# Kernel optimization log

Measured on AMD Instinct MI355X. Metric: run time of the kernel, lower is better.

Reference implementation:

```python
import jax, jax.numpy as jnp
import numpy as np

N_QUBITS = 4
N_FEATURES = 16
B = 1048576


def _bcast(theta):
    # theta: scalar or [B]; make broadcastable against [B,2,2,2] amp slices
    return theta if jnp.ndim(theta) == 0 else theta.reshape(theta.shape[0], 1, 1, 1)


def apply_ry(state, theta, w):
    # state: [B,2,2,2,2] complex; RY(theta) on wire w
    th = _bcast(theta)
    c = jnp.cos(th / 2).astype(state.dtype)
    s = jnp.sin(th / 2).astype(state.dtype)
    st = jnp.moveaxis(state, w + 1, -1)
    a0, a1 = st[..., 0], st[..., 1]
    st = jnp.stack([c * a0 - s * a1, s * a0 + c * a1], axis=-1)
    return jnp.moveaxis(st, -1, w + 1)


def apply_rz(state, theta, w):
    # RZ(theta) = diag(e^{-i theta/2}, e^{+i theta/2}) on wire w
    th = _bcast(theta)
    ph = jnp.exp(-0.5j * th.astype(jnp.float32)).astype(state.dtype)
    st = jnp.moveaxis(state, w + 1, -1)
    a0, a1 = st[..., 0], st[..., 1]
    st = jnp.stack([ph * a0, jnp.conj(ph) * a1], axis=-1)
    return jnp.moveaxis(st, -1, w + 1)


def cnot(state, c, t):
    st = jnp.moveaxis(state, (c + 1, t + 1), (-2, -1))  # [...,2(ctrl),2(tgt)]
    st = jnp.stack([st[..., 0, :], st[..., 1, ::-1]], axis=-2)
    return jnp.moveaxis(st, (-2, -1), (c + 1, t + 1))


def quantum_encoder_batched(x, qw):
    # x: [B,16] float32, qw: [8] float32 -> latents [B,4] (PauliZ expvals)
    b = x.shape[0]
    state = jnp.zeros((b, 16), jnp.complex64).at[:, 0].set(1.0)
    state = state.reshape(b, 2, 2, 2, 2)
    pi = jnp.float32(np.pi)
    for i in range(N_QUBITS):
        state = apply_ry(state, x[:, i] * pi, i)
        state = apply_rz(state, x[:, i + N_QUBITS] * pi, i)
    for i in range(N_QUBITS - 1):
        state = cnot(state, i, i + 1)
    for i in range(N_QUBITS):
        state = apply_ry(state, qw[2 * i], i)
        state = apply_rz(state, qw[2 * i + 1], i)
    for i in range(N_QUBITS - 1):
        state = cnot(state, i, i + 1)
    probs = state.real ** 2 + state.imag ** 2  # [B,2,2,2,2]
    zs = []
    for i in range(N_QUBITS):
        axes = tuple(a for a in range(1, N_QUBITS + 1) if a != i + 1)
        p = probs.sum(axes)  # [B,2]
        zs.append(p[:, 0] - p[:, 1])
    return jnp.stack(zs, axis=1)  # [B,4]


def setup_inputs() -> dict:
    key = jax.random.key(0)
    ks = jax.random.split(key, 8)
    x = jax.random.uniform(ks[0], (B, N_FEATURES), dtype=jnp.float32)
    q_weights = 0.01 * jax.random.normal(ks[1], (2 * N_QUBITS,), dtype=jnp.float32)
    # decoder: Linear(4,16) -> ReLU -> Linear(16,32) -> ReLU -> Linear(32,16)
    W1 = jax.random.normal(ks[2], (16, 4), dtype=jnp.float32) / jnp.sqrt(4.0)
    b1 = jnp.zeros((16,), jnp.float32)
    W2 = jax.random.normal(ks[3], (32, 16), dtype=jnp.float32) / jnp.sqrt(16.0)
    b2 = jnp.zeros((32,), jnp.float32)
    W3 = jax.random.normal(ks[4], (16, 32), dtype=jnp.float32) / jnp.sqrt(32.0)
    b3 = jnp.zeros((16,), jnp.float32)
    return {"x": x, "q_weights": q_weights, "W1": W1, "b1": b1,
            "W2": W2, "b2": b2, "W3": W3, "b3": b3}


def reference(x, q_weights, W1, b1, W2, b2, W3, b3):
    z = quantum_encoder_batched(x, q_weights)          # [B,4]
    h = jax.nn.relu(z @ W1.T + b1)                      # [B,16]
    h = jax.nn.relu(h @ W2.T + b2)                      # [B,32]
    return h @ W3.T + b3                                # [B,16]
```

## Files before the change

### kernel.cpp

```cpp
#include <hip/hip_runtime.h>

using u16 = unsigned short;
using u32 = unsigned int;
typedef float v2f   __attribute__((ext_vector_type(2)));
typedef float f32x4 __attribute__((ext_vector_type(4)));
typedef short s16x8 __attribute__((ext_vector_type(8)));

union FragU { u32 d[4]; s16x8 s; };

__device__ __forceinline__ u32 rne16(u32 u) { return (u + 0x7FFFu + ((u >> 16) & 1u)) >> 16; }
__device__ __forceinline__ u32 pk_bf16(float a, float b) {
    return rne16(__float_as_uint(a)) | (rne16(__float_as_uint(b)) << 16);
}
__device__ __forceinline__ void split2(float w0, float w1, u32& hi, u32& lo) {
    u32 u0 = __float_as_uint(w0), u1 = __float_as_uint(w1);
    hi = (u0 >> 16) | (u1 & 0xFFFF0000u);
    float r0 = w0 - __uint_as_float(u0 & 0xFFFF0000u);
    float r1 = w1 - __uint_as_float(u1 & 0xFFFF0000u);
    lo = pk_bf16(r0, r1);
}
__device__ __forceinline__ u32 bp(int ib, u32 v) {
    return (u32)__builtin_amdgcn_ds_bpermute(ib, (int)v);
}
__device__ __forceinline__ v2f pkfma(v2f a, v2f b, v2f c) { return __builtin_elementwise_fma(a, b, c); }
__device__ __forceinline__ v2f s2v(float x) { return (v2f){x, x}; }
__device__ __forceinline__ f32x4 tov(float4 v) { return (f32x4){v.x, v.y, v.z, v.w}; }
#define MFMA16 __builtin_amdgcn_mfma_f32_16x16x32_bf16

__global__ void __launch_bounds__(256) qae_bperm(
    const float* __restrict__ x,  const float* __restrict__ qw,
    const float* __restrict__ W1, const float* __restrict__ b1,
    const float* __restrict__ W2, const float* __restrict__ b2,
    const float* __restrict__ W3, const float* __restrict__ b3,
    float* __restrict__ out, int n)
{
    int tid  = threadIdx.x;
    int b    = blockIdx.x * 256 + tid;
    int bc   = b < n ? b : n - 1;
    int lane = tid & 63;
    int vn   = lane & 15, vq = lane >> 4;
    int gbase = blockIdx.x * 256 + (tid - lane);

    const float4* xf = reinterpret_cast<const float4*>(x);
    float4 xa = xf[(size_t)bc * 4];
    float4 xc = xf[(size_t)bc * 4 + 1];

    float th[4] = { xa.x, xa.y, xa.z, xa.w };
    float ph[4] = { xc.x, xc.y, xc.z, xc.w };
    float u0r[4], u0i[4], u1r[4], u1i[4];
    #pragma unroll
    for (int i = 0; i < 4; ++i) {
        float ct = __builtin_amdgcn_cosf(th[i] * 0.25f);
        float st = __builtin_amdgcn_sinf(th[i] * 0.25f);
        float cp = __builtin_amdgcn_cosf(ph[i] * 0.25f);
        float sp = __builtin_amdgcn_sinf(ph[i] * 0.25f);
        u0r[i] = ct * cp;  u0i[i] = -ct * sp;
        u1r[i] = st * cp;  u1i[i] = st * sp;
    }
    float p01r[4], p01i[4], p23r[4], p23i[4];
    #pragma unroll
    for (int a = 0; a < 2; ++a)
        #pragma unroll
        for (int c = 0; c < 2; ++c) {
            float arq = a ? u1r[0] : u0r[0], aiq = a ? u1i[0] : u0i[0];
            float brq = c ? u1r[1] : u0r[1], biq = c ? u1i[1] : u0i[1];
            p01r[a*2+c] = arq*brq - aiq*biq;
            p01i[a*2+c] = arq*biq + aiq*brq;
            float crq = a ? u1r[2] : u0r[2], ciq = a ? u1i[2] : u0i[2];
            float drq = c ? u1r[3] : u0r[3], diq = c ? u1i[3] : u0i[3];
            p23r[a*2+c] = crq*drq - ciq*diq;
            p23i[a*2+c] = crq*diq + ciq*drq;
        }
    v2f amp[16];
    #pragma unroll
    for (int i = 0; i < 16; ++i) {
        int q0i=(i>>3)&1, q1i=(i>>2)&1, q2i=(i>>1)&1, q3i=i&1;
        int g = (q0i<<3) | ((q1i^q0i)<<2) | ((q2i^q1i)<<1) | (q3i^q2i);
        int hi = g >> 2, lo = g & 3;
        amp[i] = (v2f){ p01r[hi]*p23r[lo] - p01i[hi]*p23i[lo],
                        p01r[hi]*p23i[lo] + p01i[hi]*p23r[lo] };
    }
    const float INV4PI = 0.07957747154594767f;
    #pragma unroll
    for (int w = 0; w < 4; ++w) {
        float a = qw[2 * w];
        v2f vc = s2v(__builtin_amdgcn_cosf(a * INV4PI));
        v2f vs = s2v(__builtin_amdgcn_sinf(a * INV4PI));
        int stride = 1 << (3 - w);
        #pragma unroll
        for (int m = 0; m < 16; ++m) {
            if (m & stride) continue;
            int i0 = m, i1 = m | stride;
            v2f a0 = amp[i0], a1 = amp[i1];
            amp[i0] = pkfma(vc, a0, -(vs * a1));
            amp[i1] = pkfma(vc, a1,  (vs * a0));
        }
    }
    float p[16];
    #pragma unroll
    for (int i = 0; i < 16; ++i) {
        int q0i=(i>>3)&1, q1i=(i>>2)&1, q2i=(i>>1)&1, q3i=i&1;
        int g = (q0i<<3) | ((q1i^q0i)<<2) | ((q2i^q1i)<<1) | (q3i^q2i);
        v2f q = amp[g] * amp[g];
        p[i] = q.x + q.y;
    }
    float s2a[8], s4[4];
    #pragma unroll
    for (int j = 0; j < 8; ++j) s2a[j] = p[2*j] + p[2*j+1];
    #pragma unroll
    for (int j = 0; j < 4; ++j) s4[j] = s2a[2*j] + s2a[2*j+1];
    float zv0 = (s4[0] + s4[1]) - (s4[2] + s4[3]);
    float zv1 = (s4[0] - s4[1]) + (s4[2] - s4[3]);
    float zv2 = (s2a[0]-s2a[1]) + (s2a[2]-s2a[3]) + (s2a[4]-s2a[5]) + (s2a[6]-s2a[7]);
    float zv3 = (p[0]-p[1]) + (p[2]-p[3]) + (p[4]-p[5]) + (p[6]-p[7])
              + (p[8]-p[9]) + (p[10]-p[11]) + (p[12]-p[13]) + (p[14]-p[15]);

    u32 zd0 = pk_bf16(zv0, zv1);
    u32 zd1 = pk_bf16(zv2, zv3);

    bool q0 = (vq == 0), qlt2 = (vq < 2);
    FragU A1h, A1l;
    {
        float4 w = reinterpret_cast<const float4*>(W1)[vn];
        u32 h0,l0,h1,l1; split2(w.x, w.y, h0, l0); split2(w.z, w.w, h1, l1);
        A1h.d[0] = q0 ? h0 : 0; A1h.d[1] = q0 ? h1 : 0; A1h.d[2] = 0; A1h.d[3] = 0;
        A1l.d[0] = q0 ? l0 : 0; A1l.d[1] = q0 ? l1 : 0; A1l.d[2] = 0; A1l.d[3] = 0;
    }
    FragU A2ah, A2al, A2bh, A2bl, A3h, A3l;
    {
        const float4* p0 = reinterpret_cast<const float4*>(W2 + vn * 16 + (vq & 1) * 8);
        const float4* p1 = reinterpret_cast<const float4*>(W2 + (16 + vn) * 16 + (vq & 1) * 8);
        float4 a0 = p0[0], a1 = p0[1], c0 = p1[0], c1 = p1[1];
        u32 h, l;
        split2(a0.x,a0.y,h,l); A2ah.d[0]=qlt2?h:0; A2al.d[0]=qlt2?l:0;
        split2(a0.z,a0.w,h,l); A2ah.d[1]=qlt2?h:0; A2al.d[1]=qlt2?l:0;
        split2(a1.x,a1.y,h,l); A2ah.d[2]=qlt2?h:0; A2al.d[2]=qlt2?l:0;
        split2(a1.z,a1.w,h,l); A2ah.d[3]=qlt2?h:0; A2al.d[3]=qlt2?l:0;
        split2(c0.x,c0.y,h,l); A2bh.d[0]=qlt2?h:0; A2bl.d[0]=qlt2?l:0;
        split2(c0.z,c0.w,h,l); A2bh.d[1]=qlt2?h:0; A2bl.d[1]=qlt2?l:0;
        split2(c1.x,c1.y,h,l); A2bh.d[2]=qlt2?h:0; A2bl.d[2]=qlt2?l:0;
        split2(c1.z,c1.w,h,l); A2bh.d[3]=qlt2?h:0; A2bl.d[3]=qlt2?l:0;
        const float4* p3 = reinterpret_cast<const float4*>(W3 + vn * 32 + vq * 8);
        float4 e0 = p3[0], e1 = p3[1];
        split2(e0.x,e0.y,h,l); A3h.d[0]=h; A3l.d[0]=l;
        split2(e0.z,e0.w,h,l); A3h.d[1]=h; A3l.d[1]=l;
        split2(e1.x,e1.y,h,l); A3h.d[2]=h; A3l.d[2]=l;
        split2(e1.z,e1.w,h,l); A3h.d[3]=h; A3l.d[3]=l;
    }
    float4 c1b = reinterpret_cast<const float4*>(b1)[vq];
    float4 c2b0 = reinterpret_cast<const float4*>(b2)[vq];
    float4 c2b1 = reinterpret_cast<const float4*>(b2)[4 + vq];
    float4 c3b = reinterpret_cast<const float4*>(b3)[vq];

    int i2a = ((((2 * vq)    ) & 3) * 16 + vn) * 4;
    int i2b = ((((2 * vq) + 1) & 3) * 16 + vn) * 4;

    #pragma unroll
    for (int t = 0; t < 4; ++t) {
        int viL = (t * 16 + vn) * 4;
        FragU B1; B1.d[0] = bp(viL, zd0); B1.d[1] = bp(viL, zd1); B1.d[2] = 0; B1.d[3] = 0;
        f32x4 c1 = tov(c1b);
        c1 = MFMA16(A1l.s, B1.s, c1, 0, 0, 0);
        c1 = MFMA16(A1h.s, B1.s, c1, 0, 0, 0);
        u32 da0 = pk_bf16(fmaxf(c1[0], 0.f), fmaxf(c1[1], 0.f));
        u32 da1 = pk_bf16(fmaxf(c1[2], 0.f), fmaxf(c1[3], 0.f));

        FragU B2;
        B2.d[0] = bp(i2a, da0); B2.d[1] = bp(i2a, da1);
        B2.d[2] = bp(i2b, da0); B2.d[3] = bp(i2b, da1);
        f32x4 ca = tov(c2b0), cb = tov(c2b1);
        ca = MFMA16(A2al.s, B2.s, ca, 0, 0, 0);
        ca = MFMA16(A2ah.s, B2.s, ca, 0, 0, 0);
        cb = MFMA16(A2bl.s, B2.s, cb, 0, 0, 0);
        cb = MFMA16(A2bh.s, B2.s, cb, 0, 0, 0);
        u32 ea0 = pk_bf16(fmaxf(ca[0],0.f), fmaxf(ca[1],0.f));
        u32 ea1 = pk_bf16(fmaxf(ca[2],0.f), fmaxf(ca[3],0.f));
        u32 eb0 = pk_bf16(fmaxf(cb[0],0.f), fmaxf(cb[1],0.f));
        u32 eb1 = pk_bf16(fmaxf(cb[2],0.f), fmaxf(cb[3],0.f));

        u32 s0a = bp(i2a, ea0), s0b = bp(i2a, eb0);
        u32 s1a = bp(i2a, ea1), s1b = bp(i2a, eb1);
        u32 s2_ = bp(i2b, ea0), s2b = bp(i2b, eb0);
        u32 s3a = bp(i2b, ea1), s3b = bp(i2b, eb1);
        FragU B3;
        B3.d[0] = qlt2 ? s0a : s0b;
        B3.d[1] = qlt2 ? s1a : s1b;
        B3.d[2] = qlt2 ? s2_ : s2b;
        B3.d[3] = qlt2 ? s3a : s3b;
        f32x4 c3 = tov(c3b);
        c3 = MFMA16(A3l.s, B3.s, c3, 0, 0, 0);
        c3 = MFMA16(A3h.s, B3.s, c3, 0, 0, 0);

        int R = gbase + t * 16 + vn;
        if (R < n)
            *reinterpret_cast<float4*>(out + (size_t)R * 16 + vq * 4) =
                make_float4(c3[0], c3[1], c3[2], c3[3]);
    }
}

extern "C" void kernel_launch(void* const* d_in, const int* in_sizes, int n_in,
                              void* d_out, int out_size, void* d_ws, size_t ws_size,
                              hipStream_t stream) {
    const float* x  = (const float*)d_in[0];
    const float* qw = (const float*)d_in[1];
    const float* W1 = (const float*)d_in[2];
    const float* b1 = (const float*)d_in[3];
    const float* W2 = (const float*)d_in[4];
    const float* b2 = (const float*)d_in[5];
    const float* W3 = (const float*)d_in[6];
    const float* b3 = (const float*)d_in[7];
    float* out = (float*)d_out;

    int n = in_sizes[0] / 16;
    int blocks = (n + 255) / 256;
    qae_bperm<<<blocks, 256, 0, stream>>>(x, qw, W1, b1, W2, b2, W3, b3, out, n);
}
```

Measured before the change: 133.7 us.

## Share weight-fragment prep via LDS, simplify encoder maths, use hardware bf16 convert

Each wave now prepares one pair of the bf16 hi/lo split weight fragments and stores them in shared memory. After a barrier every wave reads all fragments back, instead of each wave loading and splitting all weights itself. The product-state construction uses the fact that the RZ phase on |0> cancels globally, so the zero-imaginary terms are dropped. The probability reduction is done on packed v2f, and the software round-to-nearest bf16 packing is replaced with the v_cvt_pk_bf16_f32 instruction. The cost is added LDS traffic and a block-wide barrier, with some risk of small numerical differences.

Result: faster. 126.6 us (-5.3%).

```diff
diff --git a/kernel.cpp b/kernel.cpp
--- a/kernel.cpp
+++ b/kernel.cpp
@@ -6,18 +6,19 @@
 typedef float f32x4 __attribute__((ext_vector_type(4)));
 typedef short s16x8 __attribute__((ext_vector_type(8)));
 
-union FragU { u32 d[4]; s16x8 s; };
-
-__device__ __forceinline__ u32 rne16(u32 u) { return (u + 0x7FFFu + ((u >> 16) & 1u)) >> 16; }
-__device__ __forceinline__ u32 pk_bf16(float a, float b) {
-    return rne16(__float_as_uint(a)) | (rne16(__float_as_uint(b)) << 16);
+union FragU { u32 d[4]; s16x8 s; uint4 q; };
+
+__device__ __forceinline__ u32 cvt_pk_bf16(float a, float b) {
+    u32 r;
+    asm("v_cvt_pk_bf16_f32 %0, %1, %2" : "=v"(r) : "v"(a), "v"(b));
+    return r;
 }
 __device__ __forceinline__ void split2(float w0, float w1, u32& hi, u32& lo) {
     u32 u0 = __float_as_uint(w0), u1 = __float_as_uint(w1);
     hi = (u0 >> 16) | (u1 & 0xFFFF0000u);
     float r0 = w0 - __uint_as_float(u0 & 0xFFFF0000u);
     float r1 = w1 - __uint_as_float(u1 & 0xFFFF0000u);
-    lo = pk_bf16(r0, r1);
+    lo = cvt_pk_bf16(r0, r1);
 }
 __device__ __forceinline__ u32 bp(int ib, u32 v) {
     return (u32)__builtin_amdgcn_ds_bpermute(ib, (int)v);
@@ -38,47 +39,92 @@
     int b    = blockIdx.x * 256 + tid;
     int bc   = b < n ? b : n - 1;
     int lane = tid & 63;
+    int wid  = tid >> 6;
     int vn   = lane & 15, vq = lane >> 4;
     int gbase = blockIdx.x * 256 + (tid - lane);
+
+    __shared__ uint4 shfrag[8][64];
 
     const float4* xf = reinterpret_cast<const float4*>(x);
     float4 xa = xf[(size_t)bc * 4];
     float4 xc = xf[(size_t)bc * 4 + 1];
 
-    float th[4] = { xa.x, xa.y, xa.z, xa.w };
-    float ph[4] = { xc.x, xc.y, xc.z, xc.w };
-    float u0r[4], u0i[4], u1r[4], u1i[4];
+    bool q0 = (vq == 0), qlt2 = (vq < 2);
+
+    if (wid == 0) {
+        float4 w = reinterpret_cast<const float4*>(W1)[vn];
+        u32 h0, l0, h1, l1; split2(w.x, w.y, h0, l0); split2(w.z, w.w, h1, l1);
+        shfrag[0][lane] = make_uint4(q0 ? h0 : 0, q0 ? h1 : 0, 0, 0);
+        shfrag[1][lane] = make_uint4(q0 ? l0 : 0, q0 ? l1 : 0, 0, 0);
+    } else if (wid == 1) {
+        const float4* p0 = reinterpret_cast<const float4*>(W2 + vn * 16 + (vq & 1) * 8);
+        float4 a0 = p0[0], a1 = p0[1];
+        u32 h, l; uint4 H, L;
+        split2(a0.x, a0.y, h, l); H.x = qlt2 ? h : 0; L.x = qlt2 ? l : 0;
+        split2(a0.z, a0.w, h, l); H.y = qlt2 ? h : 0; L.y = qlt2 ? l : 0;
+        split2(a1.x, a1.y, h, l); H.z = qlt2 ? h : 0; L.z = qlt2 ? l : 0;
+        split2(a1.z, a1.w, h, l); H.w = qlt2 ? h : 0; L.w = qlt2 ? l : 0;
+        shfrag[2][lane] = H; shfrag[3][lane] = L;
+    } else if (wid == 2) {
+        const float4* p1 = reinterpret_cast<const float4*>(W2 + (16 + vn) * 16 + (vq & 1) * 8);
+        float4 c0 = p1[0], c1v = p1[1];
+        u32 h, l; uint4 H, L;
+        split2(c0.x, c0.y, h, l); H.x = qlt2 ? h : 0; L.x = qlt2 ? l : 0;
+        split2(c0.z, c0.w, h, l); H.y = qlt2 ? h : 0; L.y = qlt2 ? l : 0;
+        split2(c1v.x, c1v.y, h, l); H.z = qlt2 ? h : 0; L.z = qlt2 ? l : 0;
+        split2(c1v.z, c1v.w, h, l); H.w = qlt2 ? h : 0; L.w = qlt2 ? l : 0;
+        shfrag[4][lane] = H; shfrag[5][lane] = L;
+    } else {
+        const float4* p3 = reinterpret_cast<const float4*>(W3 + vn * 32 + vq * 8);
+        float4 e0 = p3[0], e1 = p3[1];
+        u32 h, l; uint4 H, L;
+        split2(e0.x, e0.y, h, l); H.x = h; L.x = l;
+        split2(e0.z, e0.w, h, l); H.y = h; L.y = l;
+        split2(e1.x, e1.y, h, l); H.z = h; L.z = l;
+        split2(e1.z, e1.w, h, l); H.w = h; L.w = l;
+        shfrag[6][lane] = H; shfrag[7][lane] = L;
+    }
+
+    float th[4]  = { xa.x, xa.y, xa.z, xa.w };
+    float phv[4] = { xc.x, xc.y, xc.z, xc.w };
+    float c4[4], u1r[4], u1i[4];
     #pragma unroll
     for (int i = 0; i < 4; ++i) {
-        float ct = __builtin_amdgcn_cosf(th[i] * 0.25f);
-        float st = __builtin_amdgcn_sinf(th[i] * 0.25f);
-        float cp = __builtin_amdgcn_cosf(ph[i] * 0.25f);
-        float sp = __builtin_amdgcn_sinf(ph[i] * 0.25f);
-        u0r[i] = ct * cp;  u0i[i] = -ct * sp;
-        u1r[i] = st * cp;  u1i[i] = st * sp;
+        float c  = __builtin_amdgcn_cosf(th[i]  * 0.25f);
+        float s  = __builtin_amdgcn_sinf(th[i]  * 0.25f);
+        float cz = __builtin_amdgcn_cosf(phv[i] * 0.5f);
+        float sz = __builtin_amdgcn_sinf(phv[i] * 0.5f);
+        c4[i] = c; u1r[i] = s * cz; u1i[i] = s * sz;
     }
     float p01r[4], p01i[4], p23r[4], p23i[4];
-    #pragma unroll
-    for (int a = 0; a < 2; ++a)
-        #pragma unroll
-        for (int c = 0; c < 2; ++c) {
-            float arq = a ? u1r[0] : u0r[0], aiq = a ? u1i[0] : u0i[0];
-            float brq = c ? u1r[1] : u0r[1], biq = c ? u1i[1] : u0i[1];
-            p01r[a*2+c] = arq*brq - aiq*biq;
-            p01i[a*2+c] = arq*biq + aiq*brq;
-            float crq = a ? u1r[2] : u0r[2], ciq = a ? u1i[2] : u0i[2];
-            float drq = c ? u1r[3] : u0r[3], diq = c ? u1i[3] : u0i[3];
-            p23r[a*2+c] = crq*drq - ciq*diq;
-            p23i[a*2+c] = crq*diq + ciq*drq;
-        }
+    p01r[0] = c4[0] * c4[1];                          p01i[0] = 0.f;
+    p01r[1] = c4[0] * u1r[1];                         p01i[1] = c4[0] * u1i[1];
+    p01r[2] = u1r[0] * c4[1];                         p01i[2] = u1i[0] * c4[1];
+    p01r[3] = u1r[0] * u1r[1] - u1i[0] * u1i[1];
+    p01i[3] = u1r[0] * u1i[1] + u1i[0] * u1r[1];
+    p23r[0] = c4[2] * c4[3];                          p23i[0] = 0.f;
+    p23r[1] = c4[2] * u1r[3];                         p23i[1] = c4[2] * u1i[3];
+    p23r[2] = u1r[2] * c4[3];                         p23i[2] = u1i[2] * c4[3];
+    p23r[3] = u1r[2] * u1r[3] - u1i[2] * u1i[3];
+    p23i[3] = u1r[2] * u1i[3] + u1i[2] * u1r[3];
+
     v2f amp[16];
     #pragma unroll
     for (int i = 0; i < 16; ++i) {
         int q0i=(i>>3)&1, q1i=(i>>2)&1, q2i=(i>>1)&1, q3i=i&1;
         int g = (q0i<<3) | ((q1i^q0i)<<2) | ((q2i^q1i)<<1) | (q3i^q2i);
         int hi = g >> 2, lo = g & 3;
-        amp[i] = (v2f){ p01r[hi]*p23r[lo] - p01i[hi]*p23i[lo],
-                        p01r[hi]*p23i[lo] + p01i[hi]*p23r[lo] };
+        float r, im;
+        if (hi == 0) {
+            if (lo == 0) { r = p01r[0] * p23r[0];  im = 0.f; }
+            else         { r = p01r[0] * p23r[lo]; im = p01r[0] * p23i[lo]; }
+        } else if (lo == 0) {
+            r = p01r[hi] * p23r[0]; im = p01i[hi] * p23r[0];
+        } else {
+            r  = p01r[hi] * p23r[lo] - p01i[hi] * p23i[lo];
+            im = p01r[hi] * p23i[lo] + p01i[hi] * p23r[lo];
+        }
+        amp[i] = (v2f){ r, im };
     }
     const float INV4PI = 0.07957747154594767f;
     #pragma unroll
@@ -96,61 +142,40 @@
             amp[i1] = pkfma(vc, a1,  (vs * a0));
         }
     }
-    float p[16];
+    v2f Pv[16];
     #pragma unroll
     for (int i = 0; i < 16; ++i) {
         int q0i=(i>>3)&1, q1i=(i>>2)&1, q2i=(i>>1)&1, q3i=i&1;
         int g = (q0i<<3) | ((q1i^q0i)<<2) | ((q2i^q1i)<<1) | (q3i^q2i);
-        v2f q = amp[g] * amp[g];
-        p[i] = q.x + q.y;
-    }
-    float s2a[8], s4[4];
-    #pragma unroll
-    for (int j = 0; j < 8; ++j) s2a[j] = p[2*j] + p[2*j+1];
-    #pragma unroll
-    for (int j = 0; j < 4; ++j) s4[j] = s2a[2*j] + s2a[2*j+1];
-    float zv0 = (s4[0] + s4[1]) - (s4[2] + s4[3]);
-    float zv1 = (s4[0] - s4[1]) + (s4[2] - s4[3]);
-    float zv2 = (s2a[0]-s2a[1]) + (s2a[2]-s2a[3]) + (s2a[4]-s2a[5]) + (s2a[6]-s2a[7]);
-    float zv3 = (p[0]-p[1]) + (p[2]-p[3]) + (p[4]-p[5]) + (p[6]-p[7])
-              + (p[8]-p[9]) + (p[10]-p[11]) + (p[12]-p[13]) + (p[14]-p[15]);
-
-    u32 zd0 = pk_bf16(zv0, zv1);
-    u32 zd1 = pk_bf16(zv2, zv3);
-
-    bool q0 = (vq == 0), qlt2 = (vq < 2);
-    FragU A1h, A1l;
-    {
-        float4 w = reinterpret_cast<const float4*>(W1)[vn];
-        u32 h0,l0,h1,l1; split2(w.x, w.y, h0, l0); split2(w.z, w.w, h1, l1);
-        A1h.d[0] = q0 ? h0 : 0; A1h.d[1] = q0 ? h1 : 0; A1h.d[2] = 0; A1h.d[3] = 0;
-        A1l.d[0] = q0 ? l0 : 0; A1l.d[1] = q0 ? l1 : 0; A1l.d[2] = 0; A1l.d[3] = 0;
-    }
-    FragU A2ah, A2al, A2bh, A2bl, A3h, A3l;
-    {
-        const float4* p0 = reinterpret_cast<const float4*>(W2 + vn * 16 + (vq & 1) * 8);
-        const float4* p1 = reinterpret_cast<const float4*>(W2 + (16 + vn) * 16 + (vq & 1) * 8);
-        float4 a0 = p0[0], a1 = p0[1], c0 = p1[0], c1 = p1[1];
-        u32 h, l;
-        split2(a0.x,a0.y,h,l); A2ah.d[0]=qlt2?h:0; A2al.d[0]=qlt2?l:0;
-        split2(a0.z,a0.w,h,l); A2ah.d[1]=qlt2?h:0; A2al.d[1]=qlt2?l:0;
-        split2(a1.x,a1.y,h,l); A2ah.d[2]=qlt2?h:0; A2al.d[2]=qlt2?l:0;
-        split2(a1.z,a1.w,h,l); A2ah.d[3]=qlt2?h:0; A2al.d[3]=qlt2?l:0;
-        split2(c0.x,c0.y,h,l); A2bh.d[0]=qlt2?h:0; A2bl.d[0]=qlt2?l:0;
-        split2(c0.z,c0.w,h,l); A2bh.d[1]=qlt2?h:0; A2bl.d[1]=qlt2?l:0;
-        split2(c1.x,c1.y,h,l); A2bh.d[2]=qlt2?h:0; A2bl.d[2]=qlt2?l:0;
-        split2(c1.z,c1.w,h,l); A2bh.d[3]=qlt2?h:0; A2bl.d[3]=qlt2?l:0;
-        const float4* p3 = reinterpret_cast<const float4*>(W3 + vn * 32 + vq * 8);
-        float4 e0 = p3[0], e1 = p3[1];
-        split2(e0.x,e0.y,h,l); A3h.d[0]=h; A3l.d[0]=l;
-        split2(e0.z,e0.w,h,l); A3h.d[1]=h; A3l.d[1]=l;
-        split2(e1.x,e1.y,h,l); A3h.d[2]=h; A3l.d[2]=l;
-        split2(e1.z,e1.w,h,l); A3h.d[3]=h; A3l.d[3]=l;
-    }
-    float4 c1b = reinterpret_cast<const float4*>(b1)[vq];
+        Pv[i] = amp[g] * amp[g];
+    }
+    v2f q2[8], q4[4];
+    #pragma unroll
+    for (int j = 0; j < 8; ++j) q2[j] = Pv[2*j] + Pv[2*j+1];
+    #pragma unroll
+    for (int j = 0; j < 4; ++j) q4[j] = q2[2*j] + q2[2*j+1];
+    v2f z0v = (q4[0] + q4[1]) - (q4[2] + q4[3]);
+    v2f z1v = (q4[0] - q4[1]) + (q4[2] - q4[3]);
+    v2f z2v = (q2[0]-q2[1]) + (q2[2]-q2[3]) + (q2[4]-q2[5]) + (q2[6]-q2[7]);
+    v2f z3v = (Pv[0]-Pv[1]) + (Pv[2]-Pv[3]) + (Pv[4]-Pv[5]) + (Pv[6]-Pv[7])
+            + (Pv[8]-Pv[9]) + (Pv[10]-Pv[11]) + (Pv[12]-Pv[13]) + (Pv[14]-Pv[15]);
+    float zv0 = z0v.x + z0v.y, zv1 = z1v.x + z1v.y;
+    float zv2 = z2v.x + z2v.y, zv3 = z3v.x + z3v.y;
+
+    u32 zd0 = cvt_pk_bf16(zv0, zv1);
+    u32 zd1 = cvt_pk_bf16(zv2, zv3);
+
+    __syncthreads();
+    FragU A1h, A1l, A2ah, A2al, A2bh, A2bl, A3h, A3l;
+    A1h.q  = shfrag[0][lane]; A1l.q  = shfrag[1][lane];
+    A2ah.q = shfrag[2][lane]; A2al.q = shfrag[3][lane];
+    A2bh.q = shfrag[4][lane]; A2bl.q = shfrag[5][lane];
+    A3h.q  = shfrag[6][lane]; A3l.q  = shfrag[7][lane];
+
+    float4 c1b  = reinterpret_cast<const float4*>(b1)[vq];
     float4 c2b0 = reinterpret_cast<const float4*>(b2)[vq];
     float4 c2b1 = reinterpret_cast<const float4*>(b2)[4 + vq];
-    float4 c3b = reinterpret_cast<const float4*>(b3)[vq];
+    float4 c3b  = reinterpret_cast<const float4*>(b3)[vq];
 
     int i2a = ((((2 * vq)    ) & 3) * 16 + vn) * 4;
     int i2b = ((((2 * vq) + 1) & 3) * 16 + vn) * 4;
@@ -162,8 +187,8 @@
         f32x4 c1 = tov(c1b);
         c1 = MFMA16(A1l.s, B1.s, c1, 0, 0, 0);
         c1 = MFMA16(A1h.s, B1.s, c1, 0, 0, 0);
-        u32 da0 = pk_bf16(fmaxf(c1[0], 0.f), fmaxf(c1[1], 0.f));
-        u32 da1 = pk_bf16(fmaxf(c1[2], 0.f), fmaxf(c1[3], 0.f));
+        u32 da0 = cvt_pk_bf16(fmaxf(c1[0], 0.f), fmaxf(c1[1], 0.f));
+        u32 da1 = cvt_pk_bf16(fmaxf(c1[2], 0.f), fmaxf(c1[3], 0.f));
 
         FragU B2;
         B2.d[0] = bp(i2a, da0); B2.d[1] = bp(i2a, da1);
@@ -173,10 +198,10 @@
         ca = MFMA16(A2ah.s, B2.s, ca, 0, 0, 0);
         cb = MFMA16(A2bl.s, B2.s, cb, 0, 0, 0);
         cb = MFMA16(A2bh.s, B2.s, cb, 0, 0, 0);
-        u32 ea0 = pk_bf16(fmaxf(ca[0],0.f), fmaxf(ca[1],0.f));
-        u32 ea1 = pk_bf16(fmaxf(ca[2],0.f), fmaxf(ca[3],0.f));
-        u32 eb0 = pk_bf16(fmaxf(cb[0],0.f), fmaxf(cb[1],0.f));
-        u32 eb1 = pk_bf16(fmaxf(cb[2],0.f), fmaxf(cb[3],0.f));
+        u32 ea0 = cvt_pk_bf16(fmaxf(ca[0],0.f), fmaxf(ca[1],0.f));
+        u32 ea1 = cvt_pk_bf16(fmaxf(ca[2],0.f), fmaxf(ca[3],0.f));
+        u32 eb0 = cvt_pk_bf16(fmaxf(cb[0],0.f), fmaxf(cb[1],0.f));
+        u32 eb1 = cvt_pk_bf16(fmaxf(cb[2],0.f), fmaxf(cb[3],0.f));
 
         u32 s0a = bp(i2a, ea0), s0b = bp(i2a, eb0);
         u32 s1a = bp(i2a, ea1), s1b = bp(i2a, eb1);
```
